# Kernel optimization log

Measured on AMD Instinct MI355X. Metric: run time of the kernel, lower is better.

## Reference

```python
import jax, jax.numpy as jnp
import numpy as np

N_EVENTS = 131072
N_FEATURES = 128
N_GLOBAL = 64
HIDDEN = 512
N_BRANCHES = 2


def setup_inputs() -> dict:
    key = jax.random.key(0)
    ks = jax.random.split(key, 4)
    x = jax.random.normal(ks[0], (N_EVENTS, N_FEATURES), dtype=jnp.float32)
    global_features = jax.random.normal(ks[1], (N_EVENTS, N_GLOBAL), dtype=jnp.float32)
    # proj_nn params: Linear(192->512) + LeakyReLU + Linear(512->256)
    W1 = jax.random.normal(ks[2], (N_FEATURES + N_GLOBAL, HIDDEN), dtype=jnp.float32) / np.sqrt(N_FEATURES + N_GLOBAL)
    b1 = jnp.zeros((HIDDEN,), dtype=jnp.float32)
    W2 = jax.random.normal(ks[3], (HIDDEN, N_BRANCHES * N_FEATURES), dtype=jnp.float32) / np.sqrt(HIDDEN)
    b2 = jnp.zeros((N_BRANCHES * N_FEATURES,), dtype=jnp.float32)
    # isplit=0: root node idxs = arange(n_events)
    parents_idxs = jnp.arange(N_EVENTS, dtype=jnp.int64 if jax.config.jax_enable_x64 else jnp.int32)
    return {"x": x, "global_features": global_features, "W1": W1, "b1": b1,
            "W2": W2, "b2": b2, "parents_idxs": parents_idxs}


def reference(x, global_features, W1, b1, W2, b2, parents_idxs):
    n_events, n_features = x.shape
    n_branches = N_BRANCHES
    n_parents = parents_idxs.shape[0] // n_events  # = 1 at isplit=0
    # gather parent node features and per-event global features
    parent_global = global_features[parents_idxs % n_events, :]   # [P*E, G]
    parents_ftxs = x[parents_idxs, :]                             # [P*E, F]
    # proj_nn: Linear -> LeakyReLU -> Linear
    h = jnp.concatenate([parents_ftxs, parent_global], axis=1)
    h = jax.nn.leaky_relu(h @ W1 + b1)                            # slope 0.01, torch default
    proj_ftx = h @ W2 + b2                                        # [P*E, B*F]
    # reshape_features: out[p, b, e] = proj[e + p*E, b*F:(b+1)*F]
    children_ftxs = (proj_ftx
                     .reshape(n_parents, n_events, n_branches, n_features)
                     .transpose(0, 2, 1, 3)
                     .reshape(n_parents * n_branches * n_events, n_features))
    return jnp.concatenate([x, children_ftxs], axis=0)
```

## Files before the change

### kernel.cpp

```cpp
#include <hip/hip_runtime.h>
#include <hip/hip_bf16.h>

#define NEV 131072
#define NF 128
#define NG 64
#define KIN 192
#define NH 512
#define NOUT 256
#define BM 64
#define NTHREADS 512

typedef __bf16 bf16x8 __attribute__((ext_vector_type(8)));
typedef __bf16 bf16x4 __attribute__((ext_vector_type(4)));
typedef float f32x4 __attribute__((ext_vector_type(4)));

__device__ __forceinline__ int a_off(int r, int cb) { return r * 384 + (cb ^ ((r & 7) << 4)); }
__device__ __forceinline__ int h_off(int r, int cb) { return r * 1024 + (cb ^ ((r & 7) << 4)); }

__global__ void pack_w(const float* __restrict__ W1, const float* __restrict__ W2,
                       __bf16* __restrict__ w1p, __bf16* __restrict__ w2p) {
    int t = blockIdx.x * blockDim.x + threadIdx.x;
    if (t < KIN * NH) {
        int j = t & 7;
        int lane = (t >> 3) & 63;
        int n = (t >> 9) & 3;
        int r = t >> 11;
        int kk = r % 6;
        int wid = r / 6;
        int lg = lane >> 4, lr = lane & 15;
        int k = kk * 32 + lg * 8 + j;
        int col = wid * 64 + n * 16 + lr;
        w1p[t] = (__bf16)W1[(size_t)k * NH + col];
    } else {
        int u = t - KIN * NH;
        if (u < NH * NOUT) {
            int j = u & 7;
            int lane = (u >> 3) & 63;
            int n = (u >> 9) & 1;
            int r = u >> 10;
            int kk = r & 15;
            int wid = r >> 4;
            int lg = lane >> 4, lr = lane & 15;
            int k = kk * 32 + lg * 8 + j;
            int col = wid * 32 + n * 16 + lr;
            w2p[u] = (__bf16)W2[(size_t)k * NOUT + col];
        }
    }
}

template <bool TW>
__global__ __launch_bounds__(NTHREADS, 2) void fused_mlp(
        const float* __restrict__ x, const float* __restrict__ gf,
        const __bf16* __restrict__ w1p, const float* __restrict__ W1f,
        const float* __restrict__ b1,
        const __bf16* __restrict__ w2p, const float* __restrict__ W2f,
        const float* __restrict__ b2,
        const int* __restrict__ idx,
        float* __restrict__ out) {
    __shared__ __align__(16) unsigned char smem[65536];

    const int tid = threadIdx.x;
    const int wid = tid >> 6;
    const int lane = tid & 63;
    const int lg = lane >> 4;
    const int lr = lane & 15;
    const int row0 = blockIdx.x * BM;

    bf16x8 b1r[KIN / 32][4];
#pragma unroll
    for (int kk = 0; kk < KIN / 32; ++kk)
#pragma unroll
        for (int n = 0; n < 4; ++n) {
            if (TW) {
                b1r[kk][n] = *(const bf16x8*)(w1p + (size_t)(((wid * 6 + kk) * 4 + n) * 64 + lane) * 8);
            } else {
                int col = wid * 64 + n * 16 + lr;
                const float* wc = W1f + (size_t)(kk * 32 + lg * 8) * NH + col;
#pragma unroll
                for (int i = 0; i < 8; ++i) b1r[kk][n][i] = (__bf16)wc[(size_t)i * NH];
            }
        }

    const f32x4* x4 = (const f32x4*)x;
    const f32x4* g4 = (const f32x4*)gf;
    f32x4* o4 = (f32x4*)out;
    for (int q = tid; q < BM * (NF / 4); q += NTHREADS) {
        int r = q >> 5, c4 = q & 31;
        int e = row0 + r;
        int p = idx[e];
        f32x4 v = x4[(size_t)e * 32 + c4];
        __builtin_nontemporal_store(v, &o4[(size_t)e * 32 + c4]);
        f32x4 vs = v;
        if (p != e) vs = x4[(size_t)p * 32 + c4];
        bf16x4 tb = {(__bf16)vs[0], (__bf16)vs[1], (__bf16)vs[2], (__bf16)vs[3]};
        *(bf16x4*)(smem + a_off(r, c4 * 8)) = tb;
    }
    for (int q = tid; q < BM * (NG / 4); q += NTHREADS) {
        int r = q >> 4, c4 = q & 15;
        int e = row0 + r;
        int p = idx[e] & (NEV - 1);
        f32x4 vs = g4[(size_t)p * 16 + c4];
        bf16x4 tb = {(__bf16)vs[0], (__bf16)vs[1], (__bf16)vs[2], (__bf16)vs[3]};
        *(bf16x4*)(smem + a_off(r, 256 + c4 * 8)) = tb;
    }
    __syncthreads();

    f32x4 acc1T[4][4] = {};
#pragma unroll
    for (int kk = 0; kk < KIN / 32; ++kk) {
        int kbyte = kk * 64 + lg * 16;
        bf16x8 a[4];
#pragma unroll
        for (int m = 0; m < 4; ++m)
            a[m] = *(const bf16x8*)(smem + a_off(m * 16 + lr, kbyte));
        __builtin_amdgcn_s_setprio(1);
#pragma unroll
        for (int n = 0; n < 4; ++n)
#pragma unroll
            for (int m = 0; m < 4; ++m)
                acc1T[n][m] = __builtin_amdgcn_mfma_f32_16x16x32_bf16(b1r[kk][n], a[m], acc1T[n][m], 0, 0, 0);
        __builtin_amdgcn_s_setprio(0);
    }

    bf16x8 b2r[NH / 32][2];
#pragma unroll
    for (int kk = 0; kk < NH / 32; ++kk)
#pragma unroll
        for (int n = 0; n < 2; ++n) {
            if (TW) {
                b2r[kk][n] = *(const bf16x8*)(w2p + (size_t)(((wid * 16 + kk) * 2 + n) * 64 + lane) * 8);
            } else {
                int col = wid * 32 + n * 16 + lr;
                const float* wc = W2f + (size_t)(kk * 32 + lg * 8) * NOUT + col;
#pragma unroll
                for (int i = 0; i < 8; ++i) b2r[kk][n][i] = (__bf16)wc[(size_t)i * NOUT];
            }
        }

    __syncthreads();

#pragma unroll
    for (int n = 0; n < 4; ++n) {
        f32x4 bb = *(const f32x4*)(b1 + wid * 64 + n * 16 + lg * 4);
        int cb = (wid * 64 + n * 16 + lg * 4) * 2;
#pragma unroll
        for (int m = 0; m < 4; ++m) {
            int e = m * 16 + lr;
            bf16x4 tb;
#pragma unroll
            for (int i = 0; i < 4; ++i) {
                float v = acc1T[n][m][i] + bb[i];
                v = (v >= 0.f) ? v : 0.01f * v;
                tb[i] = (__bf16)v;
            }
            *(bf16x4*)(smem + h_off(e, cb)) = tb;
        }
    }
    __syncthreads();

    f32x4 acc2T[2][4] = {};
#pragma unroll
    for (int kk = 0; kk < NH / 32; ++kk) {
        int kbyte = kk * 64 + lg * 16;
        bf16x8 a2[4];
#pragma unroll
        for (int m = 0; m < 4; ++m)
            a2[m] = *(const bf16x8*)(smem + h_off(m * 16 + lr, kbyte));
        __builtin_amdgcn_s_setprio(1);
#pragma unroll
        for (int n = 0; n < 2; ++n)
#pragma unroll
            for (int m = 0; m < 4; ++m)
                acc2T[n][m] = __builtin_amdgcn_mfma_f32_16x16x32_bf16(b2r[kk][n], a2[m], acc2T[n][m], 0, 0, 0);
        __builtin_amdgcn_s_setprio(0);
    }

    float* ob = out + ((size_t)NEV * (1 + (wid >> 2))) * NF;
#pragma unroll
    for (int m = 0; m < 4; ++m) {
        size_t ebase = (size_t)(row0 + m * 16 + lr) * NF;
#pragma unroll
        for (int n = 0; n < 2; ++n) {
            int col = wid * 32 + n * 16 + lg * 4;
            f32x4 bb = *(const f32x4*)(b2 + col);
            f32x4 v = acc2T[n][m] + bb;
            __builtin_nontemporal_store(v, (f32x4*)(ob + ebase + (col & 127)));
        }
    }
}

extern "C" void kernel_launch(void* const* d_in, const int* in_sizes, int n_in,
                              void* d_out, int out_size, void* d_ws, size_t ws_size,
                              hipStream_t stream) {
    const float* x  = (const float*)d_in[0];
    const float* gf = (const float*)d_in[1];
    const float* W1 = (const float*)d_in[2];
    const float* b1 = (const float*)d_in[3];
    const float* W2 = (const float*)d_in[4];
    const float* b2 = (const float*)d_in[5];
    const int*  idx = (const int*)d_in[6];
    float* out = (float*)d_out;

    const size_t wbytes = (size_t)(KIN * NH + NH * NOUT) * sizeof(__bf16);
    const int nblocks = NEV / BM;

    if (ws_size >= wbytes) {
        __bf16* w1p = (__bf16*)d_ws;
        __bf16* w2p = w1p + KIN * NH;
        int tot = KIN * NH + NH * NOUT;
        pack_w<<<(tot + 511) / 512, 512, 0, stream>>>(W1, W2, w1p, w2p);
        fused_mlp<true><<<nblocks, NTHREADS, 0, stream>>>(x, gf, w1p, nullptr, b1,
                                                          w2p, nullptr, b2, idx, out);
    } else {
        fused_mlp<false><<<nblocks, NTHREADS, 0, stream>>>(x, gf, nullptr, W1, b1,
                                                           nullptr, W2, b2, idx, out);
    }
}
```

Before: 115.7 us.

## Split fused MLP into two kernels with bf16 hidden buffer in workspace

```diff
diff --git a/kernel.cpp b/kernel.cpp
--- a/kernel.cpp
+++ b/kernel.cpp
@@ -9,6 +9,7 @@
 #define NOUT 256
 #define BM 64
 #define NTHREADS 512
+#define NBLOCKS (NEV / BM)
 
 typedef __bf16 bf16x8 __attribute__((ext_vector_type(8)));
 typedef __bf16 bf16x4 __attribute__((ext_vector_type(4)));
@@ -48,16 +49,13 @@
     }
 }
 
-template <bool TW>
-__global__ __launch_bounds__(NTHREADS, 2) void fused_mlp(
+
+__global__ __launch_bounds__(NTHREADS, 4) void k1_gemm1(
         const float* __restrict__ x, const float* __restrict__ gf,
-        const __bf16* __restrict__ w1p, const float* __restrict__ W1f,
-        const float* __restrict__ b1,
-        const __bf16* __restrict__ w2p, const float* __restrict__ W2f,
-        const float* __restrict__ b2,
+        const __bf16* __restrict__ w1p, const float* __restrict__ b1,
         const int* __restrict__ idx,
-        float* __restrict__ out) {
-    __shared__ __align__(16) unsigned char smem[65536];
+        float* __restrict__ out, __bf16* __restrict__ h) {
+    __shared__ __align__(16) unsigned char smem[24576];
 
     const int tid = threadIdx.x;
     const int wid = tid >> 6;
@@ -65,21 +63,6 @@
     const int lg = lane >> 4;
     const int lr = lane & 15;
     const int row0 = blockIdx.x * BM;
-
-    bf16x8 b1r[KIN / 32][4];
-#pragma unroll
-    for (int kk = 0; kk < KIN / 32; ++kk)
-#pragma unroll
-        for (int n = 0; n < 4; ++n) {
-            if (TW) {
-                b1r[kk][n] = *(const bf16x8*)(w1p + (size_t)(((wid * 6 + kk) * 4 + n) * 64 + lane) * 8);
-            } else {
-                int col = wid * 64 + n * 16 + lr;
-                const float* wc = W1f + (size_t)(kk * 32 + lg * 8) * NH + col;
-#pragma unroll
-                for (int i = 0; i < 8; ++i) b1r[kk][n][i] = (__bf16)wc[(size_t)i * NH];
-            }
-        }
 
     const f32x4* x4 = (const f32x4*)x;
     const f32x4* g4 = (const f32x4*)gf;
@@ -106,6 +89,183 @@
     __syncthreads();
 
     f32x4 acc1T[4][4] = {};
+    bf16x8 bcur[4], bnxt[4];
+    {
+        const __bf16* wp = w1p;
+        asm volatile("" : "+s"(wp));
+#pragma unroll
+        for (int n = 0; n < 4; ++n)
+            bcur[n] = *(const bf16x8*)(wp + (size_t)((wid * 6 + 0) * 4 + n) * 512 + lane * 8);
+    }
+#pragma unroll
+    for (int kk = 0; kk < KIN / 32; ++kk) {
+        int kbyte = kk * 64 + lg * 16;
+        bf16x8 a[4];
+#pragma unroll
+        for (int m = 0; m < 4; ++m)
+            a[m] = *(const bf16x8*)(smem + a_off(m * 16 + lr, kbyte));
+        if (kk + 1 < KIN / 32) {
+            const __bf16* wp = w1p;
+            asm volatile("" : "+s"(wp));
+#pragma unroll
+            for (int n = 0; n < 4; ++n)
+                bnxt[n] = *(const bf16x8*)(wp + (size_t)((wid * 6 + kk + 1) * 4 + n) * 512 + lane * 8);
+        }
+        __builtin_amdgcn_s_setprio(1);
+#pragma unroll
+        for (int n = 0; n < 4; ++n)
+#pragma unroll
+            for (int m = 0; m < 4; ++m)
+                acc1T[n][m] = __builtin_amdgcn_mfma_f32_16x16x32_bf16(bcur[n], a[m], acc1T[n][m], 0, 0, 0);
+        __builtin_amdgcn_s_setprio(0);
+#pragma unroll
+        for (int n = 0; n < 4; ++n) bcur[n] = bnxt[n];
+    }
+
+#pragma unroll
+    for (int n = 0; n < 4; ++n) {
+        int c0 = wid * 64 + n * 16 + lg * 4;
+        f32x4 bb = *(const f32x4*)(b1 + c0);
+        size_t fbase = (size_t)(c0 >> 5) * 512 + ((c0 >> 3) & 3) * 128 + lr * 8 + (c0 & 7);
+#pragma unroll
+        for (int m = 0; m < 4; ++m) {
+            bf16x4 tb;
+#pragma unroll
+            for (int i = 0; i < 4; ++i) {
+                float v = acc1T[n][m][i] + bb[i];
+                v = (v >= 0.f) ? v : 0.01f * v;
+                tb[i] = (__bf16)v;
+            }
+            *(bf16x4*)(h + ((size_t)(row0 >> 4) + m) * 8192 + fbase) = tb;
+        }
+    }
+}
+
+__global__ __launch_bounds__(NTHREADS, 4) void k2_gemm2(
+        const __bf16* __restrict__ h, const __bf16* __restrict__ w2p,
+        const float* __restrict__ b2, float* __restrict__ out) {
+    __shared__ __align__(16) unsigned char smem[65536];
+
+    const int tid = threadIdx.x;
+    const int wid = tid >> 6;
+    const int lane = tid & 63;
+    const int lg = lane >> 4;
+    const int lr = lane & 15;
+    const int row0 = blockIdx.x * BM;
+
+    const f32x4* h4 = (const f32x4*)(h + (size_t)row0 * NH);
+#pragma unroll
+    for (int i = 0; i < 8; ++i) {
+        f32x4 v = h4[i * NTHREADS + tid];
+        *(f32x4*)(smem + (size_t)(i * NTHREADS + tid) * 16) = v;
+    }
+    __syncthreads();
+
+    f32x4 acc2T[2][4] = {};
+    bf16x8 bcur[2], bnxt[2];
+    {
+        const __bf16* wp = w2p;
+        asm volatile("" : "+s"(wp));
+#pragma unroll
+        for (int n = 0; n < 2; ++n)
+            bcur[n] = *(const bf16x8*)(wp + (size_t)((wid * 16 + 0) * 2 + n) * 512 + lane * 8);
+    }
+#pragma unroll
+    for (int kk = 0; kk < NH / 32; ++kk) {
+        bf16x8 a2[4];
+#pragma unroll
+        for (int m = 0; m < 4; ++m)
+            a2[m] = *(const bf16x8*)(smem + m * 16384 + kk * 1024 + lg * 256 + lr * 16);
+        if (kk + 1 < NH / 32) {
+            const __bf16* wp = w2p;
+            asm volatile("" : "+s"(wp));
+#pragma unroll
+            for (int n = 0; n < 2; ++n)
+                bnxt[n] = *(const bf16x8*)(wp + (size_t)((wid * 16 + kk + 1) * 2 + n) * 512 + lane * 8);
+        }
+        __builtin_amdgcn_s_setprio(1);
+#pragma unroll
+        for (int n = 0; n < 2; ++n)
+#pragma unroll
+            for (int m = 0; m < 4; ++m)
+                acc2T[n][m] = __builtin_amdgcn_mfma_f32_16x16x32_bf16(bcur[n], a2[m], acc2T[n][m], 0, 0, 0);
+        __builtin_amdgcn_s_setprio(0);
+#pragma unroll
+        for (int n = 0; n < 2; ++n) bcur[n] = bnxt[n];
+    }
+
+    float* ob = out + ((size_t)NEV * (1 + (wid >> 2))) * NF;
+#pragma unroll
+    for (int m = 0; m < 4; ++m) {
+        size_t ebase = (size_t)(row0 + m * 16 + lr) * NF;
+#pragma unroll
+        for (int n = 0; n < 2; ++n) {
+            int col = wid * 32 + n * 16 + lg * 4;
+            f32x4 bb = *(const f32x4*)(b2 + col);
+            f32x4 v = acc2T[n][m] + bb;
+            __builtin_nontemporal_store(v, (f32x4*)(ob + ebase + (col & 127)));
+        }
+    }
+}
+
+template <bool TW>
+__global__ __launch_bounds__(NTHREADS, 2) void fused_mlp(
+        const float* __restrict__ x, const float* __restrict__ gf,
+        const __bf16* __restrict__ w1p, const float* __restrict__ W1f,
+        const float* __restrict__ b1,
+        const __bf16* __restrict__ w2p, const float* __restrict__ W2f,
+        const float* __restrict__ b2,
+        const int* __restrict__ idx,
+        float* __restrict__ out) {
+    __shared__ __align__(16) unsigned char smem[65536];
+
+    const int tid = threadIdx.x;
+    const int wid = tid >> 6;
+    const int lane = tid & 63;
+    const int lg = lane >> 4;
+    const int lr = lane & 15;
+    const int row0 = blockIdx.x * BM;
+
+    bf16x8 b1r[KIN / 32][4];
+#pragma unroll
+    for (int kk = 0; kk < KIN / 32; ++kk)
+#pragma unroll
+        for (int n = 0; n < 4; ++n) {
+            if (TW) {
+                b1r[kk][n] = *(const bf16x8*)(w1p + (size_t)(((wid * 6 + kk) * 4 + n) * 64 + lane) * 8);
+            } else {
+                int col = wid * 64 + n * 16 + lr;
+                const float* wc = W1f + (size_t)(kk * 32 + lg * 8) * NH + col;
+#pragma unroll
+                for (int i = 0; i < 8; ++i) b1r[kk][n][i] = (__bf16)wc[(size_t)i * NH];
+            }
+        }
+
+    const f32x4* x4 = (const f32x4*)x;
+    const f32x4* g4 = (const f32x4*)gf;
+    f32x4* o4 = (f32x4*)out;
+    for (int q = tid; q < BM * (NF / 4); q += NTHREADS) {
+        int r = q >> 5, c4 = q & 31;
+        int e = row0 + r;
+        int p = idx[e];
+        f32x4 v = x4[(size_t)e * 32 + c4];
+        __builtin_nontemporal_store(v, &o4[(size_t)e * 32 + c4]);
+        f32x4 vs = v;
+        if (p != e) vs = x4[(size_t)p * 32 + c4];
+        bf16x4 tb = {(__bf16)vs[0], (__bf16)vs[1], (__bf16)vs[2], (__bf16)vs[3]};
+        *(bf16x4*)(smem + a_off(r, c4 * 8)) = tb;
+    }
+    for (int q = tid; q < BM * (NG / 4); q += NTHREADS) {
+        int r = q >> 4, c4 = q & 15;
+        int e = row0 + r;
+        int p = idx[e] & (NEV - 1);
+        f32x4 vs = g4[(size_t)p * 16 + c4];
+        bf16x4 tb = {(__bf16)vs[0], (__bf16)vs[1], (__bf16)vs[2], (__bf16)vs[3]};
+        *(bf16x4*)(smem + a_off(r, 256 + c4 * 8)) = tb;
+    }
+    __syncthreads();
+
+    f32x4 acc1T[4][4] = {};
 #pragma unroll
     for (int kk = 0; kk < KIN / 32; ++kk) {
         int kbyte = kk * 64 + lg * 16;
@@ -202,17 +362,24 @@
     float* out = (float*)d_out;
 
     const size_t wbytes = (size_t)(KIN * NH + NH * NOUT) * sizeof(__bf16);
-    const int nblocks = NEV / BM;
-
-    if (ws_size >= wbytes) {
+    const size_t hbytes = (size_t)NEV * NH * sizeof(__bf16);
+    int tot = KIN * NH + NH * NOUT;
+
+    if (ws_size >= wbytes + hbytes) {
         __bf16* w1p = (__bf16*)d_ws;
         __bf16* w2p = w1p + KIN * NH;
-        int tot = KIN * NH + NH * NOUT;
+        __bf16* h   = w2p + NH * NOUT;
         pack_w<<<(tot + 511) / 512, 512, 0, stream>>>(W1, W2, w1p, w2p);
-        fused_mlp<true><<<nblocks, NTHREADS, 0, stream>>>(x, gf, w1p, nullptr, b1,
+        k1_gemm1<<<NBLOCKS, NTHREADS, 0, stream>>>(x, gf, w1p, b1, idx, out, h);
+        k2_gemm2<<<NBLOCKS, NTHREADS, 0, stream>>>(h, w2p, b2, out);
+    } else if (ws_size >= wbytes) {
+        __bf16* w1p = (__bf16*)d_ws;
+        __bf16* w2p = w1p + KIN * NH;
+        pack_w<<<(tot + 511) / 512, 512, 0, stream>>>(W1, W2, w1p, w2p);
+        fused_mlp<true><<<NBLOCKS, NTHREADS, 0, stream>>>(x, gf, w1p, nullptr, b1,
                                                           w2p, nullptr, b2, idx, out);
     } else {
-        fused_mlp<false><<<nblocks, NTHREADS, 0, stream>>>(x, gf, nullptr, W1, b1,
+        fused_mlp<false><<<NBLOCKS, NTHREADS, 0, stream>>>(x, gf, nullptr, W1, b1,
                                                            nullptr, W2, b2, idx, out);
     }
 }
```

Measured after the change: 130.8 us. 1.13x slower.
